# Optimization experiments

Measured on AMD Instinct MI355X. Metric: run time of the kernel, lower is better.

The kernel has to match this reference:

```python
import jax, jax.numpy as jnp
import numpy as np

B, S, E, H, V, L = 128, 64, 300, 512, 100000, 5


def _linear_params(k, din, dout):
    k1, k2 = jax.random.split(k)
    w = jax.random.normal(k1, (dout, din), jnp.float32) * (1.0 / np.sqrt(din))
    b = jax.random.normal(k2, (dout,), jnp.float32) * 0.01
    return w, b


def setup_inputs() -> dict:
    key = jax.random.key(0)
    ks = jax.random.split(key, 12)
    inp = {}
    inp["x"] = jax.random.randint(ks[0], (B, S), 0, V)              # word ids
    inp["bfs"] = jax.random.randint(ks[1], (B, S), 0, S)            # processing order (node index per step)
    inp["children"] = jax.random.randint(ks[2], (B, S, S), 0, 2).astype(jnp.int32)  # binary child adjacency
    inp["embed"] = jax.random.normal(ks[3], (V, E), jnp.float32) * 0.1
    names = ["ix", "ih", "fx", "fh", "ux", "uh"]
    dims = [(E, H), (H, H), (E, H), (H, H), (E, H), (H, H)]
    for n, (di, do), k in zip(names, dims, ks[4:10]):
        w, b = _linear_params(k, di, do)
        inp["W" + n] = w
        inp["b" + n] = b
    w, b = _linear_params(ks[10], H, L)
    inp["Wout"] = w
    inp["bout"] = b
    return inp


def reference(x, bfs, children, embed,
              Wix, bix, Wih, bih, Wfx, bfx, Wfh, bfh, Wux, bux, Wuh, buh,
              Wout, bout):
    # Child-Sum TreeLSTM processed in BFS order. Dropouts are eval-mode (identity).
    Bb, Ss = x.shape
    Hh = Wih.shape[0]
    xe_all = embed[x]                     # [B,S,E]
    pos = jnp.arange(Ss)

    def step(carry, cur):
        all_C, all_H, _ = carry           # all_C/all_H: [B,S,H]; cur: [B] node index this step
        xe = jnp.take_along_axis(xe_all, cur[:, None, None], axis=1)[:, 0]            # [B,E]
        cmask = jnp.take_along_axis(children, cur[:, None, None], axis=1)[:, 0]       # [B,S]
        cmask = cmask.astype(xe.dtype)
        h_sum = jnp.einsum('bs,bsh->bh', cmask, all_H)                                # sum of child hiddens
        fx_x = xe @ Wfx.T + bfx
        i = jax.nn.sigmoid(xe @ Wix.T + bix + h_sum @ Wih.T + bih)
        # NOTE: faithful to source — the 'o' gate uses fx/fh (ox/oh are dead params)
        o = jax.nn.sigmoid(fx_x + h_sum @ Wfh.T + bfh)
        u = jnp.tanh(xe @ Wux.T + bux + h_sum @ Wuh.T + buh)
        f = jax.nn.sigmoid(all_H @ Wfh.T + bfh + fx_x[:, None, :])                    # [B,S,H] per-child forget
        fc = jnp.einsum('bs,bsh->bh', cmask, f * all_C)                               # masked sum over children
        c = i * u + fc                                                                 # [B,H]
        h = o * jnp.tanh(c)
        onehot = (pos[None, :] == cur[:, None])[:, :, None]                           # [B,S,1]
        all_C = jnp.where(onehot, c[:, None, :], all_C)
        all_H = jnp.where(onehot, h[:, None, :], all_H)
        return (all_C, all_H, h), None

    init = (jnp.zeros((Bb, Ss, Hh), embed.dtype),
            jnp.zeros((Bb, Ss, Hh), embed.dtype),
            jnp.zeros((Bb, Hh), embed.dtype))
    (_, _, h_last), _ = jax.lax.scan(step, init, bfs.T)  # scan over sent_len steps
    return h_last @ Wout.T + bout                        # [B, label_num]
```

## Files before the change

kernel.cpp:

```cpp
#include <hip/hip_runtime.h>
#include <math.h>

#define BB 128
#define SS 64
#define EE 300
#define HH 512
#define LL 5
#define BSH (BB*SS*HH)
#define KP  320
#define NGRP 8
#define BPG  32
#define HSL  16
#define WSROW 520
#define HS_BASE (2*3*16*WSROW)
#define WS_BYTES ((2*3*16*WSROW + 2*16*WSROW)*2)

typedef __attribute__((ext_vector_type(8))) short bf16x8;
typedef __attribute__((ext_vector_type(4))) float f32x4;
typedef __attribute__((ext_vector_type(4))) unsigned int u32x4;

__device__ __forceinline__ float fast_sigmoid(float x) {
    return 1.0f / (1.0f + __expf(-x));
}
__device__ __forceinline__ float fast_tanh(float x) {
    x = fminf(fmaxf(x, -20.0f), 20.0f);
    float e = __expf(2.0f * x);
    return (e - 1.0f) / (e + 1.0f);
}
__device__ __forceinline__ unsigned short f2bf(float f) {
    unsigned int u = __float_as_uint(f);
    u += 0x7fffu + ((u >> 16) & 1u);
    return (unsigned short)(u >> 16);
}
__device__ __forceinline__ float bf2f(unsigned short h) {
    return __uint_as_float((unsigned int)h << 16);
}
__device__ __forceinline__ void split2(float v, unsigned short& hi, unsigned short& lo) {
    hi = f2bf(v);
    lo = f2bf(v - bf2f(hi));
}

#define LDX4V(dst, addr) \
    asm volatile("global_load_dwordx4 %0, %1, off sc0 sc1" \
                 : "=v"(dst) : "v"(addr))

#define STH(addr, val) \
    asm volatile("global_store_short %0, %1, off sc0 sc1" \
                 :: "v"(addr), "v"(val) : "memory")

__global__ __launch_bounds__(256) void prep_kernel(
    const int* __restrict__ bfs, const int* __restrict__ children,
    const float* __restrict__ Wix, const float* __restrict__ Wfx, const float* __restrict__ Wux,
    const float* __restrict__ Wih, const float* __restrict__ Wfh, const float* __restrict__ Wuh,
    unsigned short* __restrict__ Wixh, unsigned short* __restrict__ Wixl,
    unsigned short* __restrict__ Wfxh, unsigned short* __restrict__ Wfxl,
    unsigned short* __restrict__ Wuxh, unsigned short* __restrict__ Wuxl,
    unsigned short* __restrict__ Wihh, unsigned short* __restrict__ Wihl,
    unsigned short* __restrict__ Wfhh, unsigned short* __restrict__ Wfhl,
    unsigned short* __restrict__ Wuhh, unsigned short* __restrict__ Wuhl,
    unsigned char* __restrict__ clist, int* __restrict__ ccnt, int* __restrict__ bars)
{
    const int gid = blockIdx.x * 256 + threadIdx.x;
    const int G = gridDim.x * 256;
    for (int i = gid; i < NGRP * SS; i += G) bars[i] = 0;
    for (int i = gid; i < 3 * HH * KP; i += G) {
        int g = i / (HH * KP), rem = i % (HH * KP), r = rem / KP, k = rem % KP;
        const float* src = (g == 0) ? Wix : (g == 1) ? Wfx : Wux;
        unsigned short* dh = (g == 0) ? Wixh : (g == 1) ? Wfxh : Wuxh;
        unsigned short* dl = (g == 0) ? Wixl : (g == 1) ? Wfxl : Wuxl;
        float v = (k < EE) ? src[(size_t)r * EE + k] : 0.0f;
        unsigned short hi, lo; split2(v, hi, lo);
        dh[r * KP + k] = hi; dl[r * KP + k] = lo;
    }
    for (int i = gid; i < 3 * HH * HH; i += G) {
        int g = i / (HH * HH), idx = i % (HH * HH);
        const float* src = (g == 0) ? Wih : (g == 1) ? Wfh : Wuh;
        unsigned short* dh = (g == 0) ? Wihh : (g == 1) ? Wfhh : Wuhh;
        unsigned short* dl = (g == 0) ? Wihl : (g == 1) ? Wfhl : Wuhl;
        unsigned short hi, lo; split2(src[idx], hi, lo);
        dh[idx] = hi; dl[idx] = lo;
    }
    if (gid < BB * SS) {
        const int b = gid >> 6, t = gid & 63;
        unsigned long long w = 0;
        for (int tp = 0; tp < t; ++tp) w |= 1ull << (bfs[b * SS + tp] & 63);
        const int cur = bfs[b * SS + t];
        const int* crow = children + (size_t)(b * SS + cur) * SS;
        unsigned char* lst = clist + (size_t)gid * SS;
        int cnt = 0;
        for (int s = 0; s < SS; ++s)
            if (crow[s] != 0 && ((w >> s) & 1ull)) lst[cnt++] = (unsigned char)s;
        ccnt[gid] = cnt;
    }
}

__global__ __launch_bounds__(256) void xp_mfma(
    const int* __restrict__ x, const float* __restrict__ embed,
    const unsigned short* __restrict__ Wixh, const unsigned short* __restrict__ Wixl,
    const unsigned short* __restrict__ Wfxh, const unsigned short* __restrict__ Wfxl,
    const unsigned short* __restrict__ Wuxh, const unsigned short* __restrict__ Wuxl,
    const float* __restrict__ bix, const float* __restrict__ bih,
    const float* __restrict__ bfx, const float* __restrict__ bfh,
    const float* __restrict__ bux, const float* __restrict__ buh,
    float* __restrict__ XPp)
{
    const int mb = blockIdx.x;
    const int g  = blockIdx.y;
    const unsigned short* __restrict__ Wbh = (g == 0) ? Wixh : (g == 1) ? Wfxh : Wuxh;
    const unsigned short* __restrict__ Wbl = (g == 0) ? Wixl : (g == 1) ? Wfxl : Wuxl;
    const float* __restrict__ b1 = (g == 0) ? bix : (g == 1) ? bfx : bux;
    const float* __restrict__ b2 = (g == 0) ? bih : (g == 1) ? bfh : buh;

    const int row0 = mb * 16;
    __shared__ unsigned short As[2][16 * 328];
    __shared__ int toks[16];

    const int tid = threadIdx.x;
    if (tid < 16) toks[tid] = x[row0 + tid];
    __syncthreads();

    for (int i = tid; i < 16 * 75; i += 256) {
        int r = i / 75, c = i - r * 75;
        const float4 v = *(const float4*)(embed + (size_t)toks[r] * EE + c * 4);
        ushort4 hv, lv;
        split2(v.x, hv.x, lv.x); split2(v.y, hv.y, lv.y);
        split2(v.z, hv.z, lv.z); split2(v.w, hv.w, lv.w);
        *(ushort4*)&As[0][r * 328 + c * 4] = hv;
        *(ushort4*)&As[1][r * 328 + c * 4] = lv;
    }
    for (int i = tid; i < 16 * 20; i += 256) {
        int r = i / 20, k = EE + (i - r * 20);
        As[0][r * 328 + k] = 0; As[1][r * 328 + k] = 0;
    }
    __syncthreads();

    const int lane = tid & 63, wave = tid >> 6;
    const int quad = lane >> 4, col = lane & 15;
    const int wn = wave * 16;

    for (int nt = 0; nt < 8; ++nt) {
        const int gn = nt * 64 + wn + col;
        const size_t wrow = (size_t)gn * KP;
        f32x4 accA = {0.f, 0.f, 0.f, 0.f}, accB = {0.f, 0.f, 0.f, 0.f};
        #pragma unroll
        for (int kq = 0; kq < 10; ++kq) {
            const int ka = kq * 32 + quad * 8;
            bf16x8 bh = *(const bf16x8*)(Wbh + wrow + ka);
            bf16x8 bl = *(const bf16x8*)(Wbl + wrow + ka);
            bf16x8 ah = *(const bf16x8*)&As[0][col * 328 + ka];
            bf16x8 al = *(const bf16x8*)&As[1][col * 328 + ka];
            accA = __builtin_amdgcn_mfma_f32_16x16x32_bf16(ah, bh, accA, 0, 0, 0);
            accB = __builtin_amdgcn_mfma_f32_16x16x32_bf16(ah, bl, accB, 0, 0, 0);
            accA = __builtin_amdgcn_mfma_f32_16x16x32_bf16(al, bh, accA, 0, 0, 0);
        }
        const f32x4 acc = accA + accB;
        const float bb = b1[gn] + b2[gn];
        #pragma unroll
        for (int reg = 0; reg < 4; ++reg) {
            const int ml = quad * 4 + reg;
            XPp[((size_t)(row0 + ml) * HH + gn) * 4 + g] = acc[reg] + bb;
        }
    }
}

__global__ __launch_bounds__(256, 1) void fused_steps(
    const int* __restrict__ bfs, const unsigned char* __restrict__ clist,
    const int* __restrict__ ccnt, const float* __restrict__ XPp,
    const unsigned short* __restrict__ Wihh, const unsigned short* __restrict__ Wihl,
    const unsigned short* __restrict__ Wfhh, const unsigned short* __restrict__ Wfhl,
    const unsigned short* __restrict__ Wuhh, const unsigned short* __restrict__ Wuhl,
    float* __restrict__ HWC, float* __restrict__ hf32,
    unsigned short* __restrict__ h_hi, unsigned short* __restrict__ h_lo,
    int* __restrict__ bars)
{
    extern __shared__ unsigned short Ws[];
    __shared__ int s_cur[16 * 64];
    __shared__ int s_cnt[16 * 64];
    __shared__ unsigned char s_cl[16 * 64];

    const int g = blockIdx.x & 7;
    const int l = blockIdx.x >> 3;
    const int tid = threadIdx.x;
    const int m0 = g * 16;
    const int n0 = l * HSL;

    const int lane = tid & 63, wave = tid >> 6;
    const int quad = lane >> 4, col = lane & 15;

    const int chain = tid >> 4, hl = tid & 15;
    const int b = m0 + chain;
    const int h = n0 + hl;

    {
        for (int i = tid; i < 6144; i += 256) {
            const int plane = i / 3072, rem = i % 3072;
            const int gt = rem / 1024, rem2 = rem % 1024;
            const int r = rem2 >> 6, c = rem2 & 63;
            const unsigned short* src =
                (plane == 0) ? ((gt == 0) ? Wihh : (gt == 1) ? Wfhh : Wuhh)
                             : ((gt == 0) ? Wihl : (gt == 1) ? Wfhl : Wuhl);
            *(u32x4*)&Ws[((plane * 3 + gt) * 16 + r) * WSROW + c * 8] =
                *(const u32x4*)(src + (size_t)(n0 + r) * HH + c * 8);
        }
        for (int i = tid; i < 16 * 64; i += 256) {
            s_cur[i] = bfs[(m0 + (i >> 6)) * SS + (i & 63)];
            s_cnt[i] = ccnt[(m0 + (i >> 6)) * SS + (i & 63)];
        }
        if (tid < 64) {
            const int ch = tid >> 2, c = tid & 3;
            ((u32x4*)s_cl)[tid] =
                *(const u32x4*)(clist + ((size_t)(m0 + ch) * SS + 0) * SS + c * 16);
        }
    }
    __syncthreads();

    const size_t browf = (size_t)b * (SS * HH * 4);
    float4 xp_c, xp_n;
    {
        const int cur0 = s_cur[(chain << 6) + 0];
        xp_c = *(const float4*)(XPp + browf + (size_t)cur0 * (HH * 4) + h * 4);
    }

    int* gbars = bars + g * SS;

    int st_p[8], st_ch[8], st_o16[8];
    #pragma unroll
    for (int j = 0; j < 8; ++j) {
        const int i = j * 256 + tid;
        st_p[j] = i >> 10; st_ch[j] = (i & 1023) >> 6; st_o16[j] = i & 63;
    }

    for (int t = 0; t < SS; ++t) {
        const int cur = s_cur[(chain << 6) + t];
        const int cnt = s_cnt[(chain << 6) + t];
        const float xpi = xp_c.x, xpf = xp_c.y, xpu = xp_c.z;
        const float* HWb = HWC + browf + h * 4;
        const unsigned char* clp = &s_cl[chain << 6];

        float ai = 0.f, af = 0.f, au = 0.f, fc = 0.f;
        int idx = 0;
        while (idx + 8 <= cnt) {
            const float4 v0 = *(const float4*)(HWb + (size_t)clp[idx + 0] * 2048);
            const float4 v1 = *(const float4*)(HWb + (size_t)clp[idx + 1] * 2048);
            const float4 v2 = *(const float4*)(HWb + (size_t)clp[idx + 2] * 2048);
            const float4 v3 = *(const float4*)(HWb + (size_t)clp[idx + 3] * 2048);
            const float4 v4 = *(const float4*)(HWb + (size_t)clp[idx + 4] * 2048);
            const float4 v5 = *(const float4*)(HWb + (size_t)clp[idx + 5] * 2048);
            const float4 v6 = *(const float4*)(HWb + (size_t)clp[idx + 6] * 2048);
            const float4 v7 = *(const float4*)(HWb + (size_t)clp[idx + 7] * 2048);
            ai += v0.x + v1.x + v2.x + v3.x + v4.x + v5.x + v6.x + v7.x;
            af += v0.y + v1.y + v2.y + v3.y + v4.y + v5.y + v6.y + v7.y;
            au += v0.z + v1.z + v2.z + v3.z + v4.z + v5.z + v6.z + v7.z;
            fc += fast_sigmoid(v0.y + xpf) * v0.w + fast_sigmoid(v1.y + xpf) * v1.w
                + fast_sigmoid(v2.y + xpf) * v2.w + fast_sigmoid(v3.y + xpf) * v3.w
                + fast_sigmoid(v4.y + xpf) * v4.w + fast_sigmoid(v5.y + xpf) * v5.w
                + fast_sigmoid(v6.y + xpf) * v6.w + fast_sigmoid(v7.y + xpf) * v7.w;
            idx += 8;
        }
        while (idx + 4 <= cnt) {
            const float4 v0 = *(const float4*)(HWb + (size_t)clp[idx + 0] * 2048);
            const float4 v1 = *(const float4*)(HWb + (size_t)clp[idx + 1] * 2048);
            const float4 v2 = *(const float4*)(HWb + (size_t)clp[idx + 2] * 2048);
            const float4 v3 = *(const float4*)(HWb + (size_t)clp[idx + 3] * 2048);
            ai += v0.x + v1.x + v2.x + v3.x;
            af += v0.y + v1.y + v2.y + v3.y;
            au += v0.z + v1.z + v2.z + v3.z;
            fc += fast_sigmoid(v0.y + xpf) * v0.w + fast_sigmoid(v1.y + xpf) * v1.w
                + fast_sigmoid(v2.y + xpf) * v2.w + fast_sigmoid(v3.y + xpf) * v3.w;
            idx += 4;
        }
        while (idx < cnt) {
            const float4 v = *(const float4*)(HWb + (size_t)clp[idx] * 2048);
            ai += v.x; af += v.y; au += v.z;
            fc += fast_sigmoid(v.y + xpf) * v.w;
            ++idx;
        }

        const float ig = fast_sigmoid(xpi + ai);
        const float og = fast_sigmoid(xpf + af);
        const float ug = fast_tanh(xpu + au);
        const float c  = ig * ug + fc;
        const float hv = og * fast_tanh(c);

        HWC[browf + (size_t)cur * 2048 + h * 4 + 3] = c;
        if (t == SS - 1) {
            hf32[(size_t)b * HH + h] = hv;
            break;
        }
        {
            unsigned short hh_s, hlo_s; split2(hv, hh_s, hlo_s);
            const unsigned long long ah = (unsigned long long)(h_hi + (size_t)b * HH + h);
            const unsigned long long al = (unsigned long long)(h_lo + (size_t)b * HH + h);
            STH(ah, (unsigned int)hh_s);
            STH(al, (unsigned int)hlo_s);
        }
        {
            const int curn = s_cur[(chain << 6) + t + 1];
            xp_n = *(const float4*)(XPp + browf + (size_t)curn * (HH * 4) + h * 4);
        }

        __asm__ volatile("s_waitcnt vmcnt(0)" ::: "memory");
        __syncthreads();
        if (tid == 0) {
            int* cntp = gbars + t;
            __hip_atomic_fetch_add(cntp, 1, __ATOMIC_RELAXED, __HIP_MEMORY_SCOPE_AGENT);
            while (__hip_atomic_load(cntp, __ATOMIC_RELAXED, __HIP_MEMORY_SCOPE_AGENT) < BPG)
                __builtin_amdgcn_s_sleep(1);
        }
        __syncthreads();

        if (wave == 3 && lane < 64) {
            const int ch = lane >> 2, cc = lane & 3;
            ((u32x4*)s_cl)[lane] =
                *(const u32x4*)(clist + ((size_t)(m0 + ch) * SS + (t + 1)) * SS + cc * 16);
        }
        {
            u32x4 st0, st1, st2, st3, st4, st5, st6, st7;
            const unsigned long long a0 = (unsigned long long)((st_p[0] ? h_lo : h_hi) + (size_t)(m0 + st_ch[0]) * HH + st_o16[0] * 8);
            const unsigned long long a1 = (unsigned long long)((st_p[1] ? h_lo : h_hi) + (size_t)(m0 + st_ch[1]) * HH + st_o16[1] * 8);
            const unsigned long long a2 = (unsigned long long)((st_p[2] ? h_lo : h_hi) + (size_t)(m0 + st_ch[2]) * HH + st_o16[2] * 8);
            const unsigned long long a3 = (unsigned long long)((st_p[3] ? h_lo : h_hi) + (size_t)(m0 + st_ch[3]) * HH + st_o16[3] * 8);
            const unsigned long long a4 = (unsigned long long)((st_p[4] ? h_lo : h_hi) + (size_t)(m0 + st_ch[4]) * HH + st_o16[4] * 8);
            const unsigned long long a5 = (unsigned long long)((st_p[5] ? h_lo : h_hi) + (size_t)(m0 + st_ch[5]) * HH + st_o16[5] * 8);
            const unsigned long long a6 = (unsigned long long)((st_p[6] ? h_lo : h_hi) + (size_t)(m0 + st_ch[6]) * HH + st_o16[6] * 8);
            const unsigned long long a7 = (unsigned long long)((st_p[7] ? h_lo : h_hi) + (size_t)(m0 + st_ch[7]) * HH + st_o16[7] * 8);
            LDX4V(st0, a0); LDX4V(st1, a1); LDX4V(st2, a2); LDX4V(st3, a3);
            LDX4V(st4, a4); LDX4V(st5, a5); LDX4V(st6, a6); LDX4V(st7, a7);
            asm volatile("s_waitcnt vmcnt(0)" ::: "memory");
            __builtin_amdgcn_sched_barrier(0);
            *(u32x4*)&Ws[HS_BASE + (st_p[0] * 16 + st_ch[0]) * WSROW + st_o16[0] * 8] = st0;
            *(u32x4*)&Ws[HS_BASE + (st_p[1] * 16 + st_ch[1]) * WSROW + st_o16[1] * 8] = st1;
            *(u32x4*)&Ws[HS_BASE + (st_p[2] * 16 + st_ch[2]) * WSROW + st_o16[2] * 8] = st2;
            *(u32x4*)&Ws[HS_BASE + (st_p[3] * 16 + st_ch[3]) * WSROW + st_o16[3] * 8] = st3;
            *(u32x4*)&Ws[HS_BASE + (st_p[4] * 16 + st_ch[4]) * WSROW + st_o16[4] * 8] = st4;
            *(u32x4*)&Ws[HS_BASE + (st_p[5] * 16 + st_ch[5]) * WSROW + st_o16[5] * 8] = st5;
            *(u32x4*)&Ws[HS_BASE + (st_p[6] * 16 + st_ch[6]) * WSROW + st_o16[6] * 8] = st6;
            *(u32x4*)&Ws[HS_BASE + (st_p[7] * 16 + st_ch[7]) * WSROW + st_o16[7] * 8] = st7;
        }
        __syncthreads();

        if (wave < 3) {
            f32x4 accA = {0.f, 0.f, 0.f, 0.f}, accB = {0.f, 0.f, 0.f, 0.f};
            const int ha0 = HS_BASE + (0 * 16 + col) * WSROW;
            const int ha1 = HS_BASE + (1 * 16 + col) * WSROW;
            #pragma unroll
            for (int kq = 0; kq < 16; ++kq) {
                const int ka = kq * 32 + quad * 8;
                bf16x8 ahv = *(const bf16x8*)&Ws[ha0 + ka];
                bf16x8 alv = *(const bf16x8*)&Ws[ha1 + ka];
                bf16x8 bh = *(const bf16x8*)&Ws[((0 * 3 + wave) * 16 + col) * WSROW + ka];
                bf16x8 bl = *(const bf16x8*)&Ws[((1 * 3 + wave) * 16 + col) * WSROW + ka];
                accA = __builtin_amdgcn_mfma_f32_16x16x32_bf16(ahv, bh, accA, 0, 0, 0);
                accB = __builtin_amdgcn_mfma_f32_16x16x32_bf16(ahv, bl, accB, 0, 0, 0);
                accA = __builtin_amdgcn_mfma_f32_16x16x32_bf16(alv, bh, accA, 0, 0, 0);
            }
            const f32x4 acc = accA + accB;
            #pragma unroll
            for (int reg = 0; reg < 4; ++reg) {
                const int m = quad * 4 + reg;
                const int curm = s_cur[(m << 6) + t];
                HWC[(size_t)(m0 + m) * (SS * HH * 4) + (size_t)curm * 2048
                    + (n0 + col) * 4 + wave] = acc[reg];
            }
        }
        __threadfence_block();
        __syncthreads();
        xp_c = xp_n;
    }
}

__global__ __launch_bounds__(64) void out_kernel(
    const float* __restrict__ hcur,
    const float* __restrict__ Wout, const float* __restrict__ bout,
    float* __restrict__ out)
{
    const int b = blockIdx.x;
    const int lane = threadIdx.x;
    float acc[LL];
    #pragma unroll
    for (int l = 0; l < LL; ++l) acc[l] = 0.0f;
    for (int h = lane; h < HH; h += 64) {
        const float hv = hcur[(size_t)b * HH + h];
        #pragma unroll
        for (int l = 0; l < LL; ++l) acc[l] += hv * Wout[l * HH + h];
    }
    #pragma unroll
    for (int off = 32; off > 0; off >>= 1) {
        #pragma unroll
        for (int l = 0; l < LL; ++l) acc[l] += __shfl_down(acc[l], off);
    }
    if (lane == 0) {
        #pragma unroll
        for (int l = 0; l < LL; ++l) out[b * LL + l] = acc[l] + bout[l];
    }
}

extern "C" void kernel_launch(void* const* d_in, const int* in_sizes, int n_in,
                              void* d_out, int out_size, void* d_ws, size_t ws_size,
                              hipStream_t stream)
{
    (void)in_sizes; (void)n_in; (void)out_size; (void)ws_size;
    const int*   x        = (const int*)d_in[0];
    const int*   bfs      = (const int*)d_in[1];
    const int*   children = (const int*)d_in[2];
    const float* embed    = (const float*)d_in[3];
    const float* Wix = (const float*)d_in[4];
    const float* bix = (const float*)d_in[5];
    const float* Wih = (const float*)d_in[6];
    const float* bih = (const float*)d_in[7];
    const float* Wfx = (const float*)d_in[8];
    const float* bfx = (const float*)d_in[9];
    const float* Wfh = (const float*)d_in[10];
    const float* bfh = (const float*)d_in[11];
    const float* Wux = (const float*)d_in[12];
    const float* bux = (const float*)d_in[13];
    const float* Wuh = (const float*)d_in[14];
    const float* buh = (const float*)d_in[15];
    const float* Wout = (const float*)d_in[16];
    const float* bout = (const float*)d_in[17];
    float* out = (float*)d_out;

    char* p = (char*)d_ws;
    float* XPp = (float*)p;            p += (size_t)BSH * 4 * 4;
    float* HWC = (float*)p;            p += (size_t)BSH * 4 * 4;
    float* hf32 = (float*)p;           p += (size_t)BB * HH * 4;
    unsigned short* h_hi = (unsigned short*)p; p += (size_t)BB * HH * 2;
    unsigned short* h_lo = (unsigned short*)p; p += (size_t)BB * HH * 2;
    unsigned short* Wixh = (unsigned short*)p; p += (size_t)HH * KP * 2;
    unsigned short* Wixl = (unsigned short*)p; p += (size_t)HH * KP * 2;
    unsigned short* Wfxh = (unsigned short*)p; p += (size_t)HH * KP * 2;
    unsigned short* Wfxl = (unsigned short*)p; p += (size_t)HH * KP * 2;
    unsigned short* Wuxh = (unsigned short*)p; p += (size_t)HH * KP * 2;
    unsigned short* Wuxl = (unsigned short*)p; p += (size_t)HH * KP * 2;
    unsigned short* Wihh = (unsigned short*)p; p += (size_t)HH * HH * 2;
    unsigned short* Wihl = (unsigned short*)p; p += (size_t)HH * HH * 2;
    unsigned short* Wfhh = (unsigned short*)p; p += (size_t)HH * HH * 2;
    unsigned short* Wfhl = (unsigned short*)p; p += (size_t)HH * HH * 2;
    unsigned short* Wuhh = (unsigned short*)p; p += (size_t)HH * HH * 2;
    unsigned short* Wuhl = (unsigned short*)p; p += (size_t)HH * HH * 2;
    unsigned char* clist = (unsigned char*)p;  p += (size_t)BB * SS * SS;
    int* ccnt = (int*)p;               p += (size_t)BB * SS * 4;
    int* bars = (int*)p;               p += (size_t)NGRP * SS * 4;

    (void)hipFuncSetAttribute((const void*)fused_steps,
                              hipFuncAttributeMaxDynamicSharedMemorySize,
                              WS_BYTES);

    prep_kernel<<<dim3(256), 256, 0, stream>>>(
        bfs, children, Wix, Wfx, Wux, Wih, Wfh, Wuh,
        Wixh, Wixl, Wfxh, Wfxl, Wuxh, Wuxl,
        Wihh, Wihl, Wfhh, Wfhl, Wuhh, Wuhl, clist, ccnt, bars);

    xp_mfma<<<dim3(512, 3), 256, 0, stream>>>(
        x, embed, Wixh, Wixl, Wfxh, Wfxl, Wuxh, Wuxl,
        bix, bih, bfx, bfh, bux, buh, XPp);

    {
        void* args[] = {
            (void*)&bfs, (void*)&clist, (void*)&ccnt, (void*)&XPp,
            (void*)&Wihh, (void*)&Wihl, (void*)&Wfhh, (void*)&Wfhl,
            (void*)&Wuhh, (void*)&Wuhl,
            (void*)&HWC, (void*)&hf32, (void*)&h_hi, (void*)&h_lo, (void*)&bars
        };
        hipLaunchCooperativeKernel((void*)fused_steps, dim3(NGRP * BPG), dim3(256),
                                   args, WS_BYTES, stream);
    }

    out_kernel<<<dim3(BB), 64, 0, stream>>>(hf32, Wout, bout, out);
}
```

Baseline: 824.3 us.

## Precompute old-children sums while waiting on the group barrier

The setup kernel now reorders each step's child list so that the node produced by the previous step sits last, and it packs the count of already-finished children into the upper bits of ccnt. In the recurrent loop, the barrier is split into an arrive and a wait. Between them, each thread accumulates the gate sums and the forget-weighted cell sum for next step's older children, so at most one child is left to read once the barrier completes. This moves gather and sigmoid work off the critical path of the grid-wide barrier, at the cost of extra registers and an additional block sync. The LDS row padding is also bumped from 520 to 522.

```diff
diff --git a/kernel.cpp b/kernel.cpp
--- a/kernel.cpp
+++ b/kernel.cpp
@@ -11,7 +11,7 @@
 #define NGRP 8
 #define BPG  32
 #define HSL  16
-#define WSROW 520
+#define WSROW 522
 #define HS_BASE (2*3*16*WSROW)
 #define WS_BYTES ((2*3*16*WSROW + 2*16*WSROW)*2)
 
@@ -90,7 +90,19 @@
         int cnt = 0;
         for (int s = 0; s < SS; ++s)
             if (crow[s] != 0 && ((w >> s) & 1ull)) lst[cnt++] = (unsigned char)s;
-        ccnt[gid] = cnt;
+        int cold = cnt;
+        if (t > 0 && cnt > 0) {
+            const unsigned char prev = (unsigned char)bfs[b * SS + t - 1];
+            for (int i = 0; i < cnt; ++i) {
+                if (lst[i] == prev) {
+                    lst[i] = lst[cnt - 1];
+                    lst[cnt - 1] = prev;
+                    cold = cnt - 1;
+                    break;
+                }
+            }
+        }
+        ccnt[gid] = cnt | (cold << 8);
     }
 }
 
@@ -230,15 +242,18 @@
         st_p[j] = i >> 10; st_ch[j] = (i & 1023) >> 6; st_o16[j] = i & 63;
     }
 
+    float p_ai = 0.f, p_af = 0.f, p_au = 0.f, p_fc = 0.f;
+    int p_from = 0;
+
     for (int t = 0; t < SS; ++t) {
         const int cur = s_cur[(chain << 6) + t];
-        const int cnt = s_cnt[(chain << 6) + t];
+        const int cnt = s_cnt[(chain << 6) + t] & 0xff;
         const float xpi = xp_c.x, xpf = xp_c.y, xpu = xp_c.z;
         const float* HWb = HWC + browf + h * 4;
         const unsigned char* clp = &s_cl[chain << 6];
 
-        float ai = 0.f, af = 0.f, au = 0.f, fc = 0.f;
-        int idx = 0;
+        float ai = p_ai, af = p_af, au = p_au, fc = p_fc;
+        int idx = p_from;
         while (idx + 8 <= cnt) {
             const float4 v0 = *(const float4*)(HWb + (size_t)clp[idx + 0] * 2048);
             const float4 v1 = *(const float4*)(HWb + (size_t)clp[idx + 1] * 2048);
@@ -294,16 +309,46 @@
             STH(ah, (unsigned int)hh_s);
             STH(al, (unsigned int)hlo_s);
         }
+
+        __asm__ volatile("s_waitcnt vmcnt(0)" ::: "memory");
+        __syncthreads();
+
         {
             const int curn = s_cur[(chain << 6) + t + 1];
             xp_n = *(const float4*)(XPp + browf + (size_t)curn * (HH * 4) + h * 4);
         }
-
-        __asm__ volatile("s_waitcnt vmcnt(0)" ::: "memory");
-        __syncthreads();
+        if (tid == 0) {
+            __hip_atomic_fetch_add(gbars + t, 1, __ATOMIC_RELAXED, __HIP_MEMORY_SCOPE_AGENT);
+        }
+        {
+            const int pk = s_cnt[(chain << 6) + t + 1];
+            const int cold = pk >> 8;
+            const unsigned char* clg = clist + ((size_t)b * SS + (t + 1)) * SS;
+            const float xpfn = xp_n.y;
+            float ai2 = 0.f, af2 = 0.f, au2 = 0.f, fc2 = 0.f;
+            int i = 0;
+            while (i + 4 <= cold) {
+                const float4 w0 = *(const float4*)(HWb + (size_t)clg[i + 0] * 2048);
+                const float4 w1 = *(const float4*)(HWb + (size_t)clg[i + 1] * 2048);
+                const float4 w2 = *(const float4*)(HWb + (size_t)clg[i + 2] * 2048);
+                const float4 w3 = *(const float4*)(HWb + (size_t)clg[i + 3] * 2048);
+                ai2 += w0.x + w1.x + w2.x + w3.x;
+                af2 += w0.y + w1.y + w2.y + w3.y;
+                au2 += w0.z + w1.z + w2.z + w3.z;
+                fc2 += fast_sigmoid(w0.y + xpfn) * w0.w + fast_sigmoid(w1.y + xpfn) * w1.w
+                     + fast_sigmoid(w2.y + xpfn) * w2.w + fast_sigmoid(w3.y + xpfn) * w3.w;
+                i += 4;
+            }
+            while (i < cold) {
+                const float4 w = *(const float4*)(HWb + (size_t)clg[i] * 2048);
+                ai2 += w.x; af2 += w.y; au2 += w.z;
+                fc2 += fast_sigmoid(w.y + xpfn) * w.w;
+                ++i;
+            }
+            p_ai = ai2; p_af = af2; p_au = au2; p_fc = fc2; p_from = cold;
+        }
         if (tid == 0) {
             int* cntp = gbars + t;
-            __hip_atomic_fetch_add(cntp, 1, __ATOMIC_RELAXED, __HIP_MEMORY_SCOPE_AGENT);
             while (__hip_atomic_load(cntp, __ATOMIC_RELAXED, __HIP_MEMORY_SCOPE_AGENT) < BPG)
                 __builtin_amdgcn_s_sleep(1);
         }
```

Result: slower. 1.099 ms (+33.3%).
